# Optimization experiments

Measured on AMD Instinct MI355X. Metric: run time of the kernel, lower is better.

## Reference

```python
import jax, jax.numpy as jnp
import numpy as np

BATCH = 2048
OBS_DIM = 48
H0, H1, H2 = 512, 256, 128
ACT_DIM = 12
NUM_TEACHERS = 64


def setup_inputs() -> dict:
    key = jax.random.key(0)
    ks = jax.random.split(key, 10)
    s = lambda fan_in: 1.0 / np.sqrt(fan_in)
    return {
        "obs": jax.random.normal(ks[0], (BATCH, OBS_DIM), dtype=jnp.float32),
        "teacher_indices": jax.random.randint(ks[1], (BATCH,), 0, NUM_TEACHERS),
        "w0": jax.random.normal(ks[2], (NUM_TEACHERS, H0, OBS_DIM), dtype=jnp.float32) * s(OBS_DIM),
        "b0": jax.random.normal(ks[3], (NUM_TEACHERS, H0), dtype=jnp.float32) * s(OBS_DIM),
        "w2": jax.random.normal(ks[4], (NUM_TEACHERS, H1, H0), dtype=jnp.float32) * s(H0),
        "b2": jax.random.normal(ks[5], (NUM_TEACHERS, H1), dtype=jnp.float32) * s(H0),
        "w4": jax.random.normal(ks[6], (NUM_TEACHERS, H2, H1), dtype=jnp.float32) * s(H1),
        "b4": jax.random.normal(ks[7], (NUM_TEACHERS, H2), dtype=jnp.float32) * s(H1),
        "w6": jax.random.normal(ks[8], (NUM_TEACHERS, ACT_DIM, H2), dtype=jnp.float32) * s(H2),
        "b6": jax.random.normal(ks[9], (NUM_TEACHERS, ACT_DIM), dtype=jnp.float32) * s(H2),
    }


def reference(obs, teacher_indices, w0, b0, w2, b2, w4, b4, w6, b6):
    # Per-sample gather of full teacher layer weights, then batched GEMV.
    def layer(x, w, b):
        # x: [B, in]; w[idx]: [B, out, in]; b[idx]: [B, out]
        return jnp.einsum("boi,bi->bo", w[teacher_indices], x) + b[teacher_indices]

    x = jax.nn.elu(layer(obs, w0, b0))
    x = jax.nn.elu(layer(x, w2, b2))
    x = jax.nn.elu(layer(x, w4, b4))
    x = jnp.tanh(layer(x, w6, b6))
    return x
```

## Files before the change

### kernel.cpp

```cpp
#include <hip/hip_runtime.h>

#define BATCH 2048
#define NTEACH 64

typedef __attribute__((ext_vector_type(8))) short short8;
typedef __attribute__((ext_vector_type(4))) float f32x4;

__device__ __forceinline__ unsigned short f2bf(float f) {
    unsigned u = __float_as_uint(f);
    u += 0x7FFFu + ((u >> 16) & 1u);
    return (unsigned short)(u >> 16);
}

__device__ __forceinline__ short8 cvt8(float4 a, float4 b) {
    short8 r;
    r[0] = (short)f2bf(a.x); r[1] = (short)f2bf(a.y);
    r[2] = (short)f2bf(a.z); r[3] = (short)f2bf(a.w);
    r[4] = (short)f2bf(b.x); r[5] = (short)f2bf(b.y);
    r[6] = (short)f2bf(b.z); r[7] = (short)f2bf(b.w);
    return r;
}

__device__ __forceinline__ int2 wave_scan(const int* __restrict__ tidx,
                                          int t, int* ord) {
    const int lane = threadIdx.x & 63;
    int base = 0, lt = 0;
#pragma unroll
    for (int r = 0; r < 32; ++r) {
        int i = r * 64 + lane;
        int v = tidx[i];
        bool f = (v == t);
        lt += (v < t) ? 1 : 0;
        unsigned long long b = __ballot(f);
        if (ord && f) {
            int rank = base + __builtin_popcountll(b & ((1ull << lane) - 1ull));
            ord[rank] = i;
        }
        base += __builtin_popcountll(b);
    }
#pragma unroll
    for (int off = 32; off; off >>= 1) lt += __shfl_down(lt, off);
    lt = __shfl(lt, 0);
    return make_int2(lt, base);
}

__global__ __launch_bounds__(256) void l0_kernel(const float* __restrict__ obs,
                                                 const int* __restrict__ tidx,
                                                 const float* __restrict__ w0,
                                                 const float* __restrict__ b0,
                                                 int* __restrict__ offsets_g,
                                                 int* __restrict__ order_g,
                                                 unsigned short* __restrict__ h0) {
    __shared__ int ord[BATCH];
    const int t = blockIdx.y;
    const int lane = threadIdx.x & 63, wid = threadIdx.x >> 6;
    const int ln = lane & 15, kg = lane >> 4;
    const int nq = wid & 1, mq = wid >> 1;
    const int n0 = blockIdx.x * 32 + nq * 16;

    const float* wr = w0 + ((size_t)t * 512 + n0 + ln) * 48;
    bool wvalid[2];
    float4 wa[2], wb[2];
#pragma unroll
    for (int kt = 0; kt < 2; ++kt) {
        int kb = kt * 32 + kg * 8;
        wvalid[kt] = kb < 48;
        const float* p = wr + (wvalid[kt] ? kb : 0);
        wa[kt] = *(const float4*)p;
        wb[kt] = *(const float4*)(p + 4);
    }
    const float bias = b0[(size_t)t * 512 + n0 + ln];

    int2 sc = wave_scan(tidx, t, ord);
    const int start = sc.x, count = sc.y;

    if (blockIdx.x == 0) {
        if (threadIdx.x == 0) {
            offsets_g[t] = start;
            if (t == 0) offsets_g[NTEACH] = BATCH;
        }
        for (int i = threadIdx.x; i < count; i += 256) order_g[start + i] = ord[i];
    }
    if (count == 0) return;

    short8 bf[2];
#pragma unroll
    for (int kt = 0; kt < 2; ++kt) {
        short8 z = {0, 0, 0, 0, 0, 0, 0, 0};
        bf[kt] = wvalid[kt] ? cvt8(wa[kt], wb[kt]) : z;
    }

    for (int r0 = mq * 16; r0 < count; r0 += 32) {
        int lr = r0 + ln;
        const float* xr = obs + (size_t)ord[lr < count ? lr : 0] * 48;
        short8 af[2];
#pragma unroll
        for (int kt = 0; kt < 2; ++kt) {
            int kb = kt * 32 + kg * 8;
            short8 f8 = {0, 0, 0, 0, 0, 0, 0, 0};
            if (kb < 48)
                f8 = cvt8(*(const float4*)(xr + kb), *(const float4*)(xr + kb + 4));
            af[kt] = f8;
        }
        f32x4 acc = {0.f, 0.f, 0.f, 0.f};
        acc = __builtin_amdgcn_mfma_f32_16x16x32_bf16(af[0], bf[0], acc, 0, 0, 0);
        acc = __builtin_amdgcn_mfma_f32_16x16x32_bf16(af[1], bf[1], acc, 0, 0, 0);
#pragma unroll
        for (int j = 0; j < 4; ++j) {
            int row = r0 + kg * 4 + j;
            if (row < count) {
                float v = acc[j] + bias;
                v = v > 0.f ? v : expm1f(v);
                h0[(size_t)(start + row) * 512 + n0 + ln] = f2bf(v);
            }
        }
    }
}

__global__ __launch_bounds__(256) void l1_kernel(const unsigned short* __restrict__ h0,
                                                 const int* __restrict__ offsets_g,
                                                 const float* __restrict__ w2,
                                                 const float* __restrict__ b2,
                                                 unsigned short* __restrict__ h1) {
    __shared__ f32x4 red[3][64];
    const int t = blockIdx.y;
    const int start = offsets_g[t];
    const int count = offsets_g[t + 1] - start;
    if (count == 0) return;
    const int lane = threadIdx.x & 63, wid = threadIdx.x >> 6;
    const int ln = lane & 15, kg = lane >> 4;
    const int n0 = blockIdx.x * 16;
    const int kbase = wid * 128;

    short8 bf[4];
    const float* wr = w2 + ((size_t)t * 256 + n0 + ln) * 512 + kbase;
#pragma unroll
    for (int k8 = 0; k8 < 4; ++k8) {
        int kb = k8 * 32 + kg * 8;
        bf[k8] = cvt8(*(const float4*)(wr + kb), *(const float4*)(wr + kb + 4));
    }
    const float bias = b2[(size_t)t * 256 + n0 + ln];

    for (int r0 = 0; r0 < count; r0 += 16) {
        const unsigned short* xr =
            h0 + (size_t)(start + r0 + ln) * 512 + kbase + kg * 8;
        f32x4 acc = {0.f, 0.f, 0.f, 0.f};
#pragma unroll
        for (int k8 = 0; k8 < 4; ++k8)
            acc = __builtin_amdgcn_mfma_f32_16x16x32_bf16(
                *(const short8*)(xr + k8 * 32), bf[k8], acc, 0, 0, 0);
        __syncthreads();
        if (wid > 0) red[wid - 1][lane] = acc;
        __syncthreads();
        if (wid == 0) {
#pragma unroll
            for (int s = 0; s < 3; ++s) {
                f32x4 r = red[s][lane];
                acc[0] += r[0]; acc[1] += r[1]; acc[2] += r[2]; acc[3] += r[3];
            }
#pragma unroll
            for (int j = 0; j < 4; ++j) {
                int row = r0 + kg * 4 + j;
                if (row < count) {
                    float v = acc[j] + bias;
                    v = v > 0.f ? v : expm1f(v);
                    h1[(size_t)(start + row) * 256 + n0 + ln] = f2bf(v);
                }
            }
        }
    }
}

__global__ __launch_bounds__(256) void l2f_kernel(const unsigned short* __restrict__ h1,
                                                  const int* __restrict__ offsets_g,
                                                  const int* __restrict__ order_g,
                                                  const float* __restrict__ w4,
                                                  const float* __restrict__ b4,
                                                  const float* __restrict__ w6,
                                                  const float* __restrict__ b6,
                                                  float* __restrict__ out) {
    __shared__ char h2b[4096];
    const int t = blockIdx.y;
    const int start = offsets_g[t];
    const int count = offsets_g[t + 1] - start;
    if ((int)blockIdx.x * 16 >= count) return;
    const int lane = threadIdx.x & 63, wid = threadIdx.x >> 6;
    const int ln = lane & 15, kg = lane >> 4;
    const int nq = wid;

    short8 bfA[2][8];
    float biasA[2];
#pragma unroll
    for (int sub = 0; sub < 2; ++sub) {
        const float* wr = w4 + ((size_t)t * 128 + nq * 32 + sub * 16 + ln) * 256;
#pragma unroll
        for (int k8 = 0; k8 < 8; ++k8) {
            int kb = k8 * 32 + kg * 8;
            bfA[sub][k8] = cvt8(*(const float4*)(wr + kb), *(const float4*)(wr + kb + 4));
        }
        biasA[sub] = b4[(size_t)t * 128 + nq * 32 + sub * 16 + ln];
    }
    short8 bf6[4];
    float bias6 = 0.f;
    if (wid == 0) {
        const float* wr = w6 + ((size_t)t * 12 + (ln < 12 ? ln : 0)) * 128;
#pragma unroll
        for (int kt = 0; kt < 4; ++kt) {
            int kb = kt * 32 + kg * 8;
            bf6[kt] = cvt8(*(const float4*)(wr + kb), *(const float4*)(wr + kb + 4));
        }
        if (ln < 12) bias6 = b6[(size_t)t * 12 + ln];
    }

    for (int mt = blockIdx.x; mt * 16 < count; mt += gridDim.x) {
        const int gr0 = start + mt * 16;
        short8 af[8];
        const unsigned short* xr = h1 + (size_t)(gr0 + ln) * 256 + kg * 8;
#pragma unroll
        for (int k8 = 0; k8 < 8; ++k8) af[k8] = *(const short8*)(xr + k8 * 32);
#pragma unroll
        for (int sub = 0; sub < 2; ++sub) {
            f32x4 acc = {0.f, 0.f, 0.f, 0.f};
#pragma unroll
            for (int k8 = 0; k8 < 8; ++k8)
                acc = __builtin_amdgcn_mfma_f32_16x16x32_bf16(af[k8], bfA[sub][k8],
                                                              acc, 0, 0, 0);
            int col = nq * 32 + sub * 16 + ln;
#pragma unroll
            for (int j = 0; j < 4; ++j) {
                int row = kg * 4 + j;
                float v = acc[j] + biasA[sub];
                v = v > 0.f ? v : expm1f(v);
                int byte = (row * 256 + col * 2) ^ ((row & 7) << 4);
                *(unsigned short*)(h2b + byte) = f2bf(v);
            }
        }
        __syncthreads();
        if (wid == 0) {
            f32x4 acc = {0.f, 0.f, 0.f, 0.f};
#pragma unroll
            for (int kt = 0; kt < 4; ++kt) {
                int byte = (ln * 256 + (kt * 32 + kg * 8) * 2) ^ ((ln & 7) << 4);
                acc = __builtin_amdgcn_mfma_f32_16x16x32_bf16(
                    *(const short8*)(h2b + byte), bf6[kt], acc, 0, 0, 0);
            }
#pragma unroll
            for (int j = 0; j < 4; ++j) {
                int row = mt * 16 + kg * 4 + j;
                if (ln < 12 && row < count)
                    out[(size_t)order_g[start + row] * 12 + ln] = tanhf(acc[j] + bias6);
            }
        }
        __syncthreads();
    }
}

extern "C" void kernel_launch(void* const* d_in, const int* in_sizes, int n_in,
                              void* d_out, int out_size, void* d_ws, size_t ws_size,
                              hipStream_t stream) {
    const float* obs = (const float*)d_in[0];
    const int* tidx  = (const int*)d_in[1];
    const float* w0  = (const float*)d_in[2];
    const float* b0  = (const float*)d_in[3];
    const float* w2  = (const float*)d_in[4];
    const float* b2  = (const float*)d_in[5];
    const float* w4  = (const float*)d_in[6];
    const float* b4  = (const float*)d_in[7];
    const float* w6  = (const float*)d_in[8];
    const float* b6  = (const float*)d_in[9];
    float* out = (float*)d_out;

    const int ROWS = BATCH + 16;
    char* ws = (char*)d_ws;
    int* offsets = (int*)ws;
    int* order   = (int*)(ws + 1024);
    unsigned short* h0 = (unsigned short*)(ws + 16384);
    unsigned short* h1 = h0 + (size_t)ROWS * 512;

    l0_kernel<<<dim3(16, NTEACH), 256, 0, stream>>>(obs, tidx, w0, b0,
                                                    offsets, order, h0);
    l1_kernel<<<dim3(16, NTEACH), 256, 0, stream>>>(h0, offsets, w2, b2, h1);
    l2f_kernel<<<dim3(4, NTEACH), 256, 0, stream>>>(h1, offsets, order,
                                                    w4, b4, w6, b6, out);
}
```

Baseline: 42.79 us.

## Fuse layer0 and layer1 kernels, keeping h0 tile in swizzled LDS

Merges the first two layers into one kernel. Each 512-thread block recomputes the full 512-wide h0 tile for 16 rows into XOR-swizzled shared memory, then runs the layer-1 MFMA with a K-split reduction across waves. This removes the h0 round trip through global memory and one kernel launch. In exchange, each of the 8 column blocks per teacher recomputes all of layer 0, and the block adds barriers per 16-row chunk.

```diff
diff --git a/kernel.cpp b/kernel.cpp
--- a/kernel.cpp
+++ b/kernel.cpp
@@ -44,127 +44,129 @@
     return make_int2(lt, base);
 }
 
-__global__ __launch_bounds__(256) void l0_kernel(const float* __restrict__ obs,
-                                                 const int* __restrict__ tidx,
-                                                 const float* __restrict__ w0,
-                                                 const float* __restrict__ b0,
-                                                 int* __restrict__ offsets_g,
-                                                 int* __restrict__ order_g,
-                                                 unsigned short* __restrict__ h0) {
+__global__ __launch_bounds__(512, 4) void k01_kernel(
+    const float* __restrict__ obs, const int* __restrict__ tidx,
+    const float* __restrict__ w0, const float* __restrict__ b0,
+    const float* __restrict__ w2, const float* __restrict__ b2,
+    int* __restrict__ offsets_g, int* __restrict__ order_g,
+    unsigned short* __restrict__ h1) {
     __shared__ int ord[BATCH];
+    __shared__ char h0s[16384];
+    __shared__ f32x4 red[2][3][64];
+
     const int t = blockIdx.y;
-    const int lane = threadIdx.x & 63, wid = threadIdx.x >> 6;
+    const int tid = threadIdx.x;
+    const int lane = tid & 63, wid = tid >> 6;
     const int ln = lane & 15, kg = lane >> 4;
-    const int nq = wid & 1, mq = wid >> 1;
-    const int n0 = blockIdx.x * 32 + nq * 16;
-
-    const float* wr = w0 + ((size_t)t * 512 + n0 + ln) * 48;
-    bool wvalid[2];
-    float4 wa[2], wb[2];
-#pragma unroll
-    for (int kt = 0; kt < 2; ++kt) {
-        int kb = kt * 32 + kg * 8;
-        wvalid[kt] = kb < 48;
-        const float* p = wr + (wvalid[kt] ? kb : 0);
-        wa[kt] = *(const float4*)p;
-        wb[kt] = *(const float4*)(p + 4);
-    }
-    const float bias = b0[(size_t)t * 512 + n0 + ln];
+    const int a0 = wid * 64;
+    const int cg = wid >> 2, kq = wid & 3;
+    const int n0 = blockIdx.x * 32;
+
+    float4 wa[4][2], wb[4][2];
+#pragma unroll
+    for (int nt = 0; nt < 4; ++nt) {
+        const float* wr = w0 + ((size_t)t * 512 + a0 + nt * 16 + ln) * 48;
+#pragma unroll
+        for (int kt = 0; kt < 2; ++kt) {
+            int kb = kt * 32 + kg * 8;
+            const float* p = wr + (kb < 48 ? kb : 0);
+            wa[nt][kt] = *(const float4*)p;
+            wb[nt][kt] = *(const float4*)(p + 4);
+        }
+    }
+    float biasA[4];
+#pragma unroll
+    for (int nt = 0; nt < 4; ++nt)
+        biasA[nt] = b0[(size_t)t * 512 + a0 + nt * 16 + ln];
 
     int2 sc = wave_scan(tidx, t, ord);
     const int start = sc.x, count = sc.y;
 
+    short8 bf0[4][2];
+#pragma unroll
+    for (int nt = 0; nt < 4; ++nt)
+#pragma unroll
+        for (int kt = 0; kt < 2; ++kt) {
+            short8 z = {0, 0, 0, 0, 0, 0, 0, 0};
+            bf0[nt][kt] = (kt * 32 + kg * 8 < 48) ? cvt8(wa[nt][kt], wb[nt][kt]) : z;
+        }
+    const float* wr2 = w2 + ((size_t)t * 256 + n0 + cg * 16 + ln) * 512 + kq * 128;
+    float4 w2a[4], w2b[4];
+#pragma unroll
+    for (int k4 = 0; k4 < 4; ++k4) {
+        int kb = k4 * 32 + kg * 8;
+        w2a[k4] = *(const float4*)(wr2 + kb);
+        w2b[k4] = *(const float4*)(wr2 + kb + 4);
+    }
+    const float biasB = b2[(size_t)t * 256 + n0 + cg * 16 + ln];
+
     if (blockIdx.x == 0) {
-        if (threadIdx.x == 0) {
+        if (tid == 0) {
             offsets_g[t] = start;
             if (t == 0) offsets_g[NTEACH] = BATCH;
         }
-        for (int i = threadIdx.x; i < count; i += 256) order_g[start + i] = ord[i];
+        for (int i = tid; i < count; i += 512) order_g[start + i] = ord[i];
     }
     if (count == 0) return;
 
-    short8 bf[2];
-#pragma unroll
-    for (int kt = 0; kt < 2; ++kt) {
-        short8 z = {0, 0, 0, 0, 0, 0, 0, 0};
-        bf[kt] = wvalid[kt] ? cvt8(wa[kt], wb[kt]) : z;
-    }
-
-    for (int r0 = mq * 16; r0 < count; r0 += 32) {
-        int lr = r0 + ln;
-        const float* xr = obs + (size_t)ord[lr < count ? lr : 0] * 48;
-        short8 af[2];
-#pragma unroll
-        for (int kt = 0; kt < 2; ++kt) {
-            int kb = kt * 32 + kg * 8;
-            short8 f8 = {0, 0, 0, 0, 0, 0, 0, 0};
-            if (kb < 48)
-                f8 = cvt8(*(const float4*)(xr + kb), *(const float4*)(xr + kb + 4));
-            af[kt] = f8;
-        }
+    short8 bf1[4];
+#pragma unroll
+    for (int k4 = 0; k4 < 4; ++k4) bf1[k4] = cvt8(w2a[k4], w2b[k4]);
+
+    for (int c0 = 0; c0 < count; c0 += 16) {
+        __syncthreads();
+        {
+            int lr = c0 + ln;
+            const float* xr = obs + (size_t)ord[lr < count ? lr : 0] * 48;
+            short8 af[2];
+#pragma unroll
+            for (int kt = 0; kt < 2; ++kt) {
+                int kb = kt * 32 + kg * 8;
+                short8 f8 = {0, 0, 0, 0, 0, 0, 0, 0};
+                if (kb < 48)
+                    f8 = cvt8(*(const float4*)(xr + kb), *(const float4*)(xr + kb + 4));
+                af[kt] = f8;
+            }
+#pragma unroll
+            for (int nt = 0; nt < 4; ++nt) {
+                f32x4 acc = {0.f, 0.f, 0.f, 0.f};
+                acc = __builtin_amdgcn_mfma_f32_16x16x32_bf16(af[0], bf0[nt][0], acc, 0, 0, 0);
+                acc = __builtin_amdgcn_mfma_f32_16x16x32_bf16(af[1], bf0[nt][1], acc, 0, 0, 0);
+                int col = a0 + nt * 16 + ln;
+#pragma unroll
+                for (int j = 0; j < 4; ++j) {
+                    int row = kg * 4 + j;
+                    float v = acc[j] + biasA[nt];
+                    v = v > 0.f ? v : expm1f(v);
+                    int byte = (row * 1024 + col * 2) ^ ((row & 7) << 4);
+                    *(unsigned short*)(h0s + byte) = f2bf(v);
+                }
+            }
+        }
+        __syncthreads();
         f32x4 acc = {0.f, 0.f, 0.f, 0.f};
-        acc = __builtin_amdgcn_mfma_f32_16x16x32_bf16(af[0], bf[0], acc, 0, 0, 0);
-        acc = __builtin_amdgcn_mfma_f32_16x16x32_bf16(af[1], bf[1], acc, 0, 0, 0);
-#pragma unroll
-        for (int j = 0; j < 4; ++j) {
-            int row = r0 + kg * 4 + j;
-            if (row < count) {
-                float v = acc[j] + bias;
-                v = v > 0.f ? v : expm1f(v);
-                h0[(size_t)(start + row) * 512 + n0 + ln] = f2bf(v);
-            }
-        }
-    }
-}
-
-__global__ __launch_bounds__(256) void l1_kernel(const unsigned short* __restrict__ h0,
-                                                 const int* __restrict__ offsets_g,
-                                                 const float* __restrict__ w2,
-                                                 const float* __restrict__ b2,
-                                                 unsigned short* __restrict__ h1) {
-    __shared__ f32x4 red[3][64];
-    const int t = blockIdx.y;
-    const int start = offsets_g[t];
-    const int count = offsets_g[t + 1] - start;
-    if (count == 0) return;
-    const int lane = threadIdx.x & 63, wid = threadIdx.x >> 6;
-    const int ln = lane & 15, kg = lane >> 4;
-    const int n0 = blockIdx.x * 16;
-    const int kbase = wid * 128;
-
-    short8 bf[4];
-    const float* wr = w2 + ((size_t)t * 256 + n0 + ln) * 512 + kbase;
-#pragma unroll
-    for (int k8 = 0; k8 < 4; ++k8) {
-        int kb = k8 * 32 + kg * 8;
-        bf[k8] = cvt8(*(const float4*)(wr + kb), *(const float4*)(wr + kb + 4));
-    }
-    const float bias = b2[(size_t)t * 256 + n0 + ln];
-
-    for (int r0 = 0; r0 < count; r0 += 16) {
-        const unsigned short* xr =
-            h0 + (size_t)(start + r0 + ln) * 512 + kbase + kg * 8;
-        f32x4 acc = {0.f, 0.f, 0.f, 0.f};
-#pragma unroll
-        for (int k8 = 0; k8 < 4; ++k8)
+#pragma unroll
+        for (int k4 = 0; k4 < 4; ++k4) {
+            int colk = kq * 128 + k4 * 32 + kg * 8;
+            int byte = (ln * 1024 + colk * 2) ^ ((ln & 7) << 4);
             acc = __builtin_amdgcn_mfma_f32_16x16x32_bf16(
-                *(const short8*)(xr + k8 * 32), bf[k8], acc, 0, 0, 0);
-        __syncthreads();
-        if (wid > 0) red[wid - 1][lane] = acc;
-        __syncthreads();
-        if (wid == 0) {
+                *(const short8*)(h0s + byte), bf1[k4], acc, 0, 0, 0);
+        }
+        if (kq > 0) red[cg][kq - 1][lane] = acc;
+        __syncthreads();
+        if (kq == 0) {
 #pragma unroll
             for (int s = 0; s < 3; ++s) {
-                f32x4 r = red[s][lane];
+                f32x4 r = red[cg][s][lane];
                 acc[0] += r[0]; acc[1] += r[1]; acc[2] += r[2]; acc[3] += r[3];
             }
 #pragma unroll
             for (int j = 0; j < 4; ++j) {
-                int row = r0 + kg * 4 + j;
+                int row = c0 + kg * 4 + j;
                 if (row < count) {
-                    float v = acc[j] + bias;
+                    float v = acc[j] + biasB;
                     v = v > 0.f ? v : expm1f(v);
-                    h1[(size_t)(start + row) * 256 + n0 + ln] = f2bf(v);
+                    h1[(size_t)(start + row) * 256 + n0 + cg * 16 + ln] = f2bf(v);
                 }
             }
         }
@@ -274,12 +276,10 @@
     char* ws = (char*)d_ws;
     int* offsets = (int*)ws;
     int* order   = (int*)(ws + 1024);
-    unsigned short* h0 = (unsigned short*)(ws + 16384);
-    unsigned short* h1 = h0 + (size_t)ROWS * 512;
-
-    l0_kernel<<<dim3(16, NTEACH), 256, 0, stream>>>(obs, tidx, w0, b0,
-                                                    offsets, order, h0);
-    l1_kernel<<<dim3(16, NTEACH), 256, 0, stream>>>(h0, offsets, w2, b2, h1);
+    unsigned short* h1 = (unsigned short*)(ws + 16384);
+
+    k01_kernel<<<dim3(8, NTEACH), 512, 0, stream>>>(obs, tidx, w0, b0, w2, b2,
+                                                    offsets, order, h1);
     l2f_kernel<<<dim3(4, NTEACH), 256, 0, stream>>>(h1, offsets, order,
                                                     w4, b4, w6, b6, out);
 }
```

Result: slower. 48.32 us (+12.9%).
